# Kernel tuning notes

Measured on AMD Instinct MI355X. Metric: run time of the kernel, lower is better.

The kernel has to match this reference:

```python
import jax, jax.numpy as jnp
import numpy as np

N = 10000      # nodes
E = 160000     # edges
D = 512        # hidden = input channels (residual requires equality)
OUT = 128      # output channels
G = 64         # graphs in batch


def setup_inputs() -> dict:
    key = jax.random.key(0)
    ks = jax.random.split(key, 16)
    s = 1.0 / np.sqrt(D)
    inp = {
        "x": jax.random.normal(ks[0], (N, D), jnp.float32) * 0.1,
        "edge_index": jax.random.randint(ks[1], (2, E), 0, N, dtype=jnp.int64),
        "batch": jnp.sort(jax.random.randint(ks[2], (N,), 0, G, dtype=jnp.int64)),
    }
    for i in range(5):
        inp[f"Wr{i+1}"] = jax.random.uniform(ks[3 + 2 * i], (D, D), jnp.float32, -s, s)  # lin_rel weight
        inp[f"Ws{i+1}"] = jax.random.uniform(ks[4 + 2 * i], (D, D), jnp.float32, -s, s)  # lin_root weight (no bias)
        inp[f"b{i+1}"] = jnp.zeros((D,), jnp.float32)                                     # lin_rel bias
    inp["Wlin"] = jax.random.uniform(ks[13], (D, OUT), jnp.float32, -s, s)
    inp["blin"] = jnp.zeros((OUT,), jnp.float32)
    return inp


def graph_conv(x, src, dst, Wr, Ws, b):
    # PyG GraphConv(aggr='add'): out = lin_rel(sum_{j in N(i)} x_j) + lin_root(x_i)
    agg = jax.ops.segment_sum(x[src], dst, num_segments=N)  # [N, D] scatter-add
    return agg @ Wr + b + x @ Ws


def reference(x, Wr1, Ws1, b1, Wr2, Ws2, b2, Wr3, Ws3, b3, Wr4, Ws4, b4, Wr5, Ws5, b5, Wlin, blin, edge_index, batch):
    src, dst = edge_index[0], edge_index[1]
    x = jax.nn.relu(x + graph_conv(x, src, dst, Wr1, Ws1, b1))
    x = jax.nn.relu(x + graph_conv(x, src, dst, Wr2, Ws2, b2))
    x = jax.nn.relu(x + graph_conv(x, src, dst, Wr3, Ws3, b3))
    x = jax.nn.relu(x + graph_conv(x, src, dst, Wr4, Ws4, b4))
    x = x + graph_conv(x, src, dst, Wr5, Ws5, b5)  # no relu after conv5
    # global_mean_pool over graph ids
    sums = jax.ops.segment_sum(x, batch, num_segments=G)                       # [G, D]
    cnt = jax.ops.segment_sum(jnp.ones((N, 1), x.dtype), batch, num_segments=G)
    x = sums / jnp.maximum(cnt, 1.0)
    return x @ Wlin + blin  # [G, OUT]
```

## Files before the change

kernel.cpp:

```cpp
#include <hip/hip_runtime.h>
#include <hip/hip_bf16.h>

#define NN 10000
#define EE 160000
#define DD 512
#define GG 64
#define OUTC 128
#define NBLK 628

typedef __attribute__((ext_vector_type(8))) short bf16x8;
typedef __attribute__((ext_vector_type(4))) float f32x4;

static __device__ __forceinline__ unsigned short f2bf(float f) {
  unsigned u = __builtin_bit_cast(unsigned, f);
  unsigned rounding = 0x7fffu + ((u >> 16) & 1u);
  u += rounding;
  return (unsigned short)(u >> 16);
}

static __device__ __forceinline__ void gload_lds16(const void* g, void* l) {
  __builtin_amdgcn_global_load_lds(
      (const __attribute__((address_space(1))) unsigned*)g,
      (__attribute__((address_space(3))) unsigned*)l, 16, 0, 0);
}

__global__ void hist_dst(const int* __restrict__ dst, int* __restrict__ cnt) {
  int e = blockIdx.x * 256 + threadIdx.x;
  if (e < EE) atomicAdd(&cnt[dst[e]], 1);
}

__global__ void scan_offsets(const int* __restrict__ cnt, int* __restrict__ offs) {
  __shared__ int wpre[17];
  __shared__ int carry;
  int t = threadIdx.x;
  int lane = t & 63, wv = t >> 6;
  if (t == 0) carry = 0;
  __syncthreads();
  for (int base = 0; base < NN; base += 1024) {
    int i = base + t;
    int v = (i < NN) ? cnt[i] : 0;
    int s = v;
#pragma unroll
    for (int d = 1; d < 64; d <<= 1) {
      int o = __shfl_up(s, d, 64);
      if (lane >= d) s += o;
    }
    if (lane == 63) wpre[wv] = s;
    __syncthreads();
    if (t == 0) {
      int r = 0;
      for (int w = 0; w < 16; ++w) { int x = wpre[w]; wpre[w] = r; r += x; }
      wpre[16] = r;
    }
    __syncthreads();
    int incl = s + wpre[wv] + carry;
    if (i < NN) offs[i] = incl - v;
    __syncthreads();
    if (t == 0) carry += wpre[16];
    __syncthreads();
  }
  if (t == 0) offs[NN] = carry;
}

__global__ void fill_edges(const int* __restrict__ src, const int* __restrict__ dst,
                           const int* __restrict__ offs, int* __restrict__ fptr,
                           int* __restrict__ ssrc) {
  int e = blockIdx.x * 256 + threadIdx.x;
  if (e < EE) {
    int d = dst[e];
    int p = atomicAdd(&fptr[d], 1);
    ssrc[offs[d] + p] = src[e];
  }
}

struct WPtrs { const float* p[10]; };

__global__ void transpose_w_all(WPtrs wp, unsigned short* __restrict__ WT) {
  __shared__ float tile[32][33];
  int z = blockIdx.z;
  const float* W = wp.p[z];
  unsigned short* dst = WT + (size_t)(z >> 1) * DD * 1024 + (size_t)(z & 1) * DD;
  int bx = blockIdx.x * 32, by = blockIdx.y * 32;
  int tx = threadIdx.x, ty = threadIdx.y;
  for (int i = ty; i < 32; i += 8)
    tile[i][tx] = W[(size_t)(by + i) * DD + bx + tx];
  __syncthreads();
  int addI = z & 1;
  for (int i = ty; i < 32; i += 8) {
    float v = tile[tx][i];
    if (addI && (by + tx) == (bx + i)) v += 1.0f;
    dst[(size_t)(bx + i) * 1024 + by + tx] = f2bf(v);
  }
}

__global__ void convert_x(const float* __restrict__ x, unsigned short* __restrict__ m0) {
  int i = blockIdx.x * 256 + threadIdx.x;
  if (i < NN * DD / 2) {
    float2 v = ((const float2*)x)[i];
    unsigned u = (unsigned)f2bf(v.x) | ((unsigned)f2bf(v.y) << 16);
    int e = i << 1;
    int row = e >> 9, col = e & 511;
    ((unsigned*)m0)[row * 512 + 256 + (col >> 1)] = u;
  }
}

static __device__ __forceinline__ void acc8(float* a, uint4 v) {
  unsigned w0 = v.x, w1 = v.y, w2 = v.z, w3 = v.w;
  a[0] += __builtin_bit_cast(float, w0 << 16);
  a[1] += __builtin_bit_cast(float, w0 & 0xffff0000u);
  a[2] += __builtin_bit_cast(float, w1 << 16);
  a[3] += __builtin_bit_cast(float, w1 & 0xffff0000u);
  a[4] += __builtin_bit_cast(float, w2 << 16);
  a[5] += __builtin_bit_cast(float, w2 & 0xffff0000u);
  a[6] += __builtin_bit_cast(float, w3 << 16);
  a[7] += __builtin_bit_cast(float, w3 & 0xffff0000u);
}

__global__ __launch_bounds__(256) void seg_sum(unsigned short* __restrict__ merged,
                                               const int* __restrict__ offs,
                                               const int* __restrict__ ssrc) {
  int node = (blockIdx.x << 2) + (threadIdx.x >> 6);
  if (node >= NN) return;
  int lane = threadIdx.x & 63;
  int beg = offs[node], end = offs[node + 1];
  const uint4* xb = (const uint4*)merged;
  float a[8] = {0.f, 0.f, 0.f, 0.f, 0.f, 0.f, 0.f, 0.f};
  int e = beg;
  for (; e + 8 <= end; e += 8) {
    uint4 v0 = xb[(size_t)ssrc[e] * 128 + 64 + lane];
    uint4 v1 = xb[(size_t)ssrc[e + 1] * 128 + 64 + lane];
    uint4 v2 = xb[(size_t)ssrc[e + 2] * 128 + 64 + lane];
    uint4 v3 = xb[(size_t)ssrc[e + 3] * 128 + 64 + lane];
    uint4 v4 = xb[(size_t)ssrc[e + 4] * 128 + 64 + lane];
    uint4 v5 = xb[(size_t)ssrc[e + 5] * 128 + 64 + lane];
    uint4 v6 = xb[(size_t)ssrc[e + 6] * 128 + 64 + lane];
    uint4 v7 = xb[(size_t)ssrc[e + 7] * 128 + 64 + lane];
    acc8(a, v0); acc8(a, v1); acc8(a, v2); acc8(a, v3);
    acc8(a, v4); acc8(a, v5); acc8(a, v6); acc8(a, v7);
  }
  for (; e + 4 <= end; e += 4) {
    uint4 v0 = xb[(size_t)ssrc[e] * 128 + 64 + lane];
    uint4 v1 = xb[(size_t)ssrc[e + 1] * 128 + 64 + lane];
    uint4 v2 = xb[(size_t)ssrc[e + 2] * 128 + 64 + lane];
    uint4 v3 = xb[(size_t)ssrc[e + 3] * 128 + 64 + lane];
    acc8(a, v0); acc8(a, v1); acc8(a, v2); acc8(a, v3);
  }
  for (; e < end; ++e) {
    uint4 v = xb[(size_t)ssrc[e] * 128 + 64 + lane];
    acc8(a, v);
  }
  uint4 o;
  o.x = (unsigned)f2bf(a[0]) | ((unsigned)f2bf(a[1]) << 16);
  o.y = (unsigned)f2bf(a[2]) | ((unsigned)f2bf(a[3]) << 16);
  o.z = (unsigned)f2bf(a[4]) | ((unsigned)f2bf(a[5]) << 16);
  o.w = (unsigned)f2bf(a[6]) | ((unsigned)f2bf(a[7]) << 16);
  ((uint4*)merged)[(size_t)node * 128 + lane] = o;
}

__global__ __launch_bounds__(256) void gemm_layer(
    const unsigned short* __restrict__ Am,
    const unsigned short* __restrict__ Bw,
    const float* __restrict__ bias,
    unsigned short* __restrict__ xout,
    int do_relu) {
  __shared__ unsigned short Al[2][64 * 64];
  __shared__ unsigned short Bl[2][128 * 64];
  int tid = threadIdx.x;
  int lane = tid & 63, wave = tid >> 6;
  int wr = wave >> 1, wc = wave & 1;

  int orig = blockIdx.x;
  int xcd = orig & 7, cidx = orig >> 3;
  int wgid = (xcd < 4) ? xcd * 79 + cidx : 316 + (xcd - 4) * 78 + cidx;
  int brow = (wgid >> 2) * 64;
  int bcol = (wgid & 3) * 128;
  int lrow = lane & 15, lq = lane >> 4;

  f32x4 acc[2][4];
#pragma unroll
  for (int m = 0; m < 2; ++m)
#pragma unroll
    for (int n = 0; n < 4; ++n) acc[m][n] = (f32x4){0.f, 0.f, 0.f, 0.f};

  auto STAGE = [&](int buf, int t) {
    int k0 = t * 64;
#pragma unroll
    for (int i = 0; i < 2; ++i) {
      int idx = i * 256 + tid;
      int row = idx >> 3, c = idx & 7;
      int csw = (c ^ (row & 7)) * 8;
      int gr = brow + row;
      if (gr >= NN) gr = NN - 1;
      gload_lds16(Am + (size_t)gr * 1024 + k0 + csw, &Al[buf][idx * 8]);
    }
#pragma unroll
    for (int i = 0; i < 4; ++i) {
      int idx = i * 256 + tid;
      int row = idx >> 3, c = idx & 7;
      int csw = (c ^ (row & 7)) * 8;
      gload_lds16(Bw + (size_t)(bcol + row) * 1024 + k0 + csw, &Bl[buf][idx * 8]);
    }
  };

  STAGE(0, 0);
  __syncthreads();
  int cur = 0;
#pragma unroll 1
  for (int t = 0; t < 16; ++t) {
    if (t < 15) STAGE(cur ^ 1, t + 1);
#pragma unroll
    for (int kk = 0; kk < 2; ++kk) {
      bf16x8 a[2], b[4];
      int lc = kk * 4 + lq;
#pragma unroll
      for (int m = 0; m < 2; ++m) {
        int row = wr * 32 + m * 16 + lrow;
        a[m] = *(const bf16x8*)&Al[cur][row * 64 + ((lc ^ (lrow & 7)) * 8)];
      }
#pragma unroll
      for (int n = 0; n < 4; ++n) {
        int row = wc * 64 + n * 16 + lrow;
        b[n] = *(const bf16x8*)&Bl[cur][row * 64 + ((lc ^ (lrow & 7)) * 8)];
      }
#pragma unroll
      for (int m = 0; m < 2; ++m)
#pragma unroll
        for (int n = 0; n < 4; ++n)
          acc[m][n] = __builtin_amdgcn_mfma_f32_16x16x32_bf16(a[m], b[n], acc[m][n], 0, 0, 0);
    }
    __syncthreads();
    cur ^= 1;
  }

  int crow = lq * 4, ccol = lrow;
#pragma unroll
  for (int m = 0; m < 2; ++m) {
#pragma unroll
    for (int n = 0; n < 4; ++n) {
      int col = bcol + wc * 64 + n * 16 + ccol;
      float bv = bias[col];
#pragma unroll
      for (int i = 0; i < 4; ++i) {
        int row = brow + wr * 32 + m * 16 + crow + i;
        if (row < NN) {
          float v = acc[m][n][i] + bv;
          if (do_relu) v = fmaxf(v, 0.f);
          xout[(size_t)row * 1024 + 512 + col] = f2bf(v);
        }
      }
    }
  }
}

__global__ void graph_bounds(const int* __restrict__ batch, int* __restrict__ gstart) {
  int i = blockIdx.x * 256 + threadIdx.x;
  if (i >= NN) return;
  int cur = batch[i];
  int prev = (i == 0) ? -1 : batch[i - 1];
  for (int g = prev + 1; g <= cur; ++g) gstart[g] = i;
  if (i == NN - 1)
    for (int g = cur + 1; g <= GG; ++g) gstart[g] = NN;
}

__global__ __launch_bounds__(256) void pool_partial(const unsigned short* __restrict__ mfin,
                                                    const int* __restrict__ gstart,
                                                    float* __restrict__ pooled) {
  int g = blockIdx.x, part = blockIdx.y;
  int t = threadIdx.x;
  int beg = gstart[g], end = gstart[g + 1];
  int n = end - beg;
  int per = (n + 7) >> 3;
  int b = beg + part * per;
  int e = b + per; if (e > end) e = end;
  if (b >= e) return;
  const unsigned* mw = (const unsigned*)mfin;
  float a0 = 0.f, a1 = 0.f;
  for (int r = b; r < e; ++r) {
    unsigned v = mw[(size_t)r * 512 + 256 + t];
    a0 += __builtin_bit_cast(float, v << 16);
    a1 += __builtin_bit_cast(float, v & 0xffff0000u);
  }
  atomicAdd(&pooled[g * DD + 2 * t], a0);
  atomicAdd(&pooled[g * DD + 2 * t + 1], a1);
}

__global__ __launch_bounds__(128) void final_linear(const float* __restrict__ pooled,
                                                    const int* __restrict__ gstart,
                                                    const float* __restrict__ Wlin,
                                                    const float* __restrict__ blin,
                                                    float* __restrict__ out) {
  __shared__ float p[128];
  int g = blockIdx.x, kq = blockIdx.y;
  int o = threadIdx.x;
  int cnt = gstart[g + 1] - gstart[g];
  float inv = 1.0f / fmaxf((float)cnt, 1.0f);
  p[o] = pooled[g * DD + kq * 128 + o] * inv;
  __syncthreads();
  float s = (kq == 0) ? blin[o] : 0.f;
#pragma unroll 8
  for (int k = 0; k < 128; ++k)
    s += p[k] * Wlin[(size_t)(kq * 128 + k) * OUTC + o];
  atomicAdd(&out[g * OUTC + o], s);
}

extern "C" void kernel_launch(void* const* d_in, const int* in_sizes, int n_in,
                              void* d_out, int out_size, void* d_ws, size_t ws_size,
                              hipStream_t stream) {
  const float* x_in = (const float*)d_in[0];
  const int* ei = (const int*)d_in[1];
  const int* src = ei;
  const int* dst = ei + EE;
  const int* batch = (const int*)d_in[2];
  WPtrs wp;
  const float* bias[5];
  for (int l = 0; l < 5; ++l) {
    wp.p[2 * l] = (const float*)d_in[3 + 3 * l];
    wp.p[2 * l + 1] = (const float*)d_in[4 + 3 * l];
    bias[l] = (const float*)d_in[5 + 3 * l];
  }
  const float* Wlin = (const float*)d_in[18];
  const float* blin = (const float*)d_in[19];
  float* out = (float*)d_out;

  char* ws = (char*)d_ws;
  size_t off = 0;
  auto alloc = [&](size_t bytes) { size_t o = off; off += (bytes + 511) & ~(size_t)511; return o; };
  unsigned short* m0 = (unsigned short*)(ws + alloc((size_t)NN * 1024 * 2));
  unsigned short* m1 = (unsigned short*)(ws + alloc((size_t)NN * 1024 * 2));
  unsigned short* wt = (unsigned short*)(ws + alloc((size_t)5 * DD * 1024 * 2));
  int* deg = (int*)(ws + alloc((size_t)2 * NN * 4));
  int* fptr = deg + NN;
  int* offs = (int*)(ws + alloc((size_t)(NN + 1) * 4));
  int* ssrc = (int*)(ws + alloc((size_t)EE * 4));
  int* gstart = (int*)(ws + alloc((size_t)(GG + 1) * 4));
  float* pooled = (float*)(ws + alloc((size_t)GG * DD * 4));

  hipMemsetAsync(deg, 0, (size_t)2 * NN * 4, stream);
  hipMemsetAsync(pooled, 0, (size_t)GG * DD * 4, stream);
  hipMemsetAsync(out, 0, (size_t)GG * OUTC * 4, stream);

  int eblocks = (EE + 255) / 256;
  hist_dst<<<eblocks, 256, 0, stream>>>(dst, deg);
  scan_offsets<<<1, 1024, 0, stream>>>(deg, offs);
  fill_edges<<<eblocks, 256, 0, stream>>>(src, dst, offs, fptr, ssrc);

  dim3 tb(32, 8), tg(DD / 32, DD / 32, 10);
  transpose_w_all<<<tg, tb, 0, stream>>>(wp, wt);

  convert_x<<<(NN * DD / 2 + 255) / 256, 256, 0, stream>>>(x_in, m0);

  graph_bounds<<<(NN + 255) / 256, 256, 0, stream>>>(batch, gstart);

  unsigned short* mc = m0;
  unsigned short* mn = m1;
  for (int l = 0; l < 5; ++l) {
    seg_sum<<<(NN + 3) / 4, 256, 0, stream>>>(mc, offs, ssrc);
    gemm_layer<<<NBLK, 256, 0, stream>>>(mc, wt + (size_t)l * DD * 1024,
                                         bias[l], mn, l < 4 ? 1 : 0);
    unsigned short* t = mc; mc = mn; mn = t;
  }

  dim3 pgrid(GG, 8);
  pool_partial<<<pgrid, 256, 0, stream>>>(mc, gstart, pooled);
  dim3 fgrid(GG, 4);
  final_linear<<<fgrid, 128, 0, stream>>>(pooled, gstart, Wlin, blin, out);
}
```

Measured before the change: 273.1 us.

## Slice segment-sum by feature columns with XCD-aware block mapping

Replaces the per-node 16-byte-per-lane gather kernel with a sliced version where each block handles one 128-column slice (4-byte loads per lane) for four nodes. Block IDs are mapped so that blocks landing on the same XCD work on the same column slice, which shrinks the working set each XCD's L2 has to cache for the random neighbour gathers. The cost is four times as many blocks, narrower loads, and the edge index list being re-read once per slice.

```diff
diff --git a/kernel.cpp b/kernel.cpp
--- a/kernel.cpp
+++ b/kernel.cpp
@@ -104,57 +104,43 @@
   }
 }
 
-static __device__ __forceinline__ void acc8(float* a, uint4 v) {
-  unsigned w0 = v.x, w1 = v.y, w2 = v.z, w3 = v.w;
-  a[0] += __builtin_bit_cast(float, w0 << 16);
-  a[1] += __builtin_bit_cast(float, w0 & 0xffff0000u);
-  a[2] += __builtin_bit_cast(float, w1 << 16);
-  a[3] += __builtin_bit_cast(float, w1 & 0xffff0000u);
-  a[4] += __builtin_bit_cast(float, w2 << 16);
-  a[5] += __builtin_bit_cast(float, w2 & 0xffff0000u);
-  a[6] += __builtin_bit_cast(float, w3 << 16);
-  a[7] += __builtin_bit_cast(float, w3 & 0xffff0000u);
-}
-
-__global__ __launch_bounds__(256) void seg_sum(unsigned short* __restrict__ merged,
-                                               const int* __restrict__ offs,
-                                               const int* __restrict__ ssrc) {
-  int node = (blockIdx.x << 2) + (threadIdx.x >> 6);
-  if (node >= NN) return;
-  int lane = threadIdx.x & 63;
+__global__ __launch_bounds__(256) void seg_sum_sliced(unsigned short* __restrict__ merged,
+                                                      const int* __restrict__ offs,
+                                                      const int* __restrict__ ssrc) {
+  int bid = blockIdx.x;
+  int s8 = bid & 7;
+  int g = bid >> 3;
+  int slice = s8 & 3, sub = s8 >> 2;
+  int wave = threadIdx.x >> 6, lane = threadIdx.x & 63;
+  int node = (sub * 1250 + g) * 4 + wave;
   int beg = offs[node], end = offs[node + 1];
-  const uint4* xb = (const uint4*)merged;
-  float a[8] = {0.f, 0.f, 0.f, 0.f, 0.f, 0.f, 0.f, 0.f};
+  const unsigned* xw = (const unsigned*)merged;
+  int co = 256 + slice * 64 + lane;
+  float a0 = 0.f, a1 = 0.f;
   int e = beg;
+#define SEG_LD(i) unsigned v##i = xw[(size_t)ssrc[e + i] * 512 + co]
+#define SEG_AC(i)                                          \
+  a0 += __builtin_bit_cast(float, v##i << 16);             \
+  a1 += __builtin_bit_cast(float, v##i & 0xffff0000u)
   for (; e + 8 <= end; e += 8) {
-    uint4 v0 = xb[(size_t)ssrc[e] * 128 + 64 + lane];
-    uint4 v1 = xb[(size_t)ssrc[e + 1] * 128 + 64 + lane];
-    uint4 v2 = xb[(size_t)ssrc[e + 2] * 128 + 64 + lane];
-    uint4 v3 = xb[(size_t)ssrc[e + 3] * 128 + 64 + lane];
-    uint4 v4 = xb[(size_t)ssrc[e + 4] * 128 + 64 + lane];
-    uint4 v5 = xb[(size_t)ssrc[e + 5] * 128 + 64 + lane];
-    uint4 v6 = xb[(size_t)ssrc[e + 6] * 128 + 64 + lane];
-    uint4 v7 = xb[(size_t)ssrc[e + 7] * 128 + 64 + lane];
-    acc8(a, v0); acc8(a, v1); acc8(a, v2); acc8(a, v3);
-    acc8(a, v4); acc8(a, v5); acc8(a, v6); acc8(a, v7);
+    SEG_LD(0); SEG_LD(1); SEG_LD(2); SEG_LD(3);
+    SEG_LD(4); SEG_LD(5); SEG_LD(6); SEG_LD(7);
+    SEG_AC(0); SEG_AC(1); SEG_AC(2); SEG_AC(3);
+    SEG_AC(4); SEG_AC(5); SEG_AC(6); SEG_AC(7);
   }
   for (; e + 4 <= end; e += 4) {
-    uint4 v0 = xb[(size_t)ssrc[e] * 128 + 64 + lane];
-    uint4 v1 = xb[(size_t)ssrc[e + 1] * 128 + 64 + lane];
-    uint4 v2 = xb[(size_t)ssrc[e + 2] * 128 + 64 + lane];
-    uint4 v3 = xb[(size_t)ssrc[e + 3] * 128 + 64 + lane];
-    acc8(a, v0); acc8(a, v1); acc8(a, v2); acc8(a, v3);
+    SEG_LD(0); SEG_LD(1); SEG_LD(2); SEG_LD(3);
+    SEG_AC(0); SEG_AC(1); SEG_AC(2); SEG_AC(3);
   }
   for (; e < end; ++e) {
-    uint4 v = xb[(size_t)ssrc[e] * 128 + 64 + lane];
-    acc8(a, v);
-  }
-  uint4 o;
-  o.x = (unsigned)f2bf(a[0]) | ((unsigned)f2bf(a[1]) << 16);
-  o.y = (unsigned)f2bf(a[2]) | ((unsigned)f2bf(a[3]) << 16);
-  o.z = (unsigned)f2bf(a[4]) | ((unsigned)f2bf(a[5]) << 16);
-  o.w = (unsigned)f2bf(a[6]) | ((unsigned)f2bf(a[7]) << 16);
-  ((uint4*)merged)[(size_t)node * 128 + lane] = o;
+    unsigned v = xw[(size_t)ssrc[e] * 512 + co];
+    a0 += __builtin_bit_cast(float, v << 16);
+    a1 += __builtin_bit_cast(float, v & 0xffff0000u);
+  }
+#undef SEG_LD
+#undef SEG_AC
+  unsigned o = (unsigned)f2bf(a0) | ((unsigned)f2bf(a1) << 16);
+  ((unsigned*)merged)[(size_t)node * 512 + slice * 64 + lane] = o;
 }
 
 __global__ __launch_bounds__(256) void gemm_layer(
@@ -354,7 +340,7 @@
   unsigned short* mc = m0;
   unsigned short* mn = m1;
   for (int l = 0; l < 5; ++l) {
-    seg_sum<<<(NN + 3) / 4, 256, 0, stream>>>(mc, offs, ssrc);
+    seg_sum_sliced<<<10000, 256, 0, stream>>>(mc, offs, ssrc);
     gemm_layer<<<NBLK, 256, 0, stream>>>(mc, wt + (size_t)l * DD * 1024,
                                          bias[l], mn, l < 4 ? 1 : 0);
     unsigned short* t = mc; mc = mn; mn = t;
```

Result: faster. 266.8 us (-2.3%).
